# Kernel tuning notes

Measured on AMD Instinct MI355X. Metric: run time of the kernel, lower is better.

Reference implementation:

```python
import jax, jax.numpy as jnp
import numpy as np

N_NODES = 100000
N_EDGES = 1600000
D_IN = 128
D_HID = 128
D_OUT = 16


def gcn_conv(x, W, b, src, dst, deg_inv_sqrt, deg_inv):
    # PyG GCNConv: transform then normalized aggregate with self-loops.
    h = x @ W  # [N, H]
    norm = deg_inv_sqrt[src] * deg_inv_sqrt[dst]  # [E]
    msg = h[src] * norm[:, None]  # [E, H] gather
    agg = jax.ops.segment_sum(msg, dst, num_segments=N_NODES)  # scatter-add
    agg = agg + h * deg_inv[:, None]  # self-loop term (weight deg^-1)
    return agg + b


def setup_inputs() -> dict:
    key = jax.random.key(0)
    ks = jax.random.split(key, 10)
    x = jax.random.normal(ks[0], (N_NODES, D_IN), dtype=jnp.float32)
    edge_index = jax.random.randint(ks[1], (2, N_EDGES), 0, N_NODES)
    s = 1.0 / np.sqrt(D_IN)
    sh = 1.0 / np.sqrt(D_HID)
    W0 = jax.random.uniform(ks[2], (D_IN, D_HID), jnp.float32, -s, s)
    b0 = jnp.zeros((D_HID,), jnp.float32)
    W1 = jax.random.uniform(ks[3], (D_HID, D_HID), jnp.float32, -sh, sh)
    b1 = jnp.zeros((D_HID,), jnp.float32)
    W2 = jax.random.uniform(ks[4], (D_HID, D_HID), jnp.float32, -sh, sh)
    b2 = jnp.zeros((D_HID,), jnp.float32)
    Wr = jax.random.uniform(ks[5], (D_HID, D_OUT), jnp.float32, -sh, sh)
    br = jax.random.uniform(ks[6], (D_OUT,), jnp.float32, -sh, sh)
    return {"x": x, "edge_index": edge_index, "W0": W0, "b0": b0,
            "W1": W1, "b1": b1, "W2": W2, "b2": b2, "Wr": Wr, "br": br}


def reference(x, edge_index, W0, b0, W1, b1, W2, b2, Wr, br):
    src, dst = edge_index[0], edge_index[1]
    # degree with self-loops: deg[i] = 1 + indegree(i)
    deg = jax.ops.segment_sum(jnp.ones((N_EDGES,), x.dtype), dst,
                              num_segments=N_NODES) + 1.0
    deg_inv_sqrt = deg ** -0.5
    deg_inv = 1.0 / deg
    h = x
    for W, b in ((W0, b0), (W1, b1), (W2, b2)):
        h = gcn_conv(h, W, b, src, dst, deg_inv_sqrt, deg_inv)
        h = jax.nn.relu(h)  # dropout is identity at inference
    out = h @ Wr + br
    return jax.nn.sigmoid(out) * 0.8 + 0.1
```

## Files before the change

### kernel.cpp

```cpp
#include <hip/hip_runtime.h>
#include <math.h>

#define N_NODES 100000
#define N_EDGES 1600000
#define NBUCKET 782
#define EB      256
#define EPB     6250

typedef __attribute__((ext_vector_type(8))) __bf16 bf16x8;
typedef __attribute__((ext_vector_type(4))) float  f32x4;


static __device__ __forceinline__ unsigned short f2bf(float f) {
    unsigned int u = __float_as_uint(f);
    unsigned int r = (u + 0x7FFFu + ((u >> 16) & 1u)) >> 16;
    return (unsigned short)r;
}
static __device__ __forceinline__ float bf2f(unsigned short h) {
    return __uint_as_float(((unsigned int)h) << 16);
}


__global__ __launch_bounds__(256) void xconv_kernel(const float* __restrict__ X,
                                                    unsigned short* __restrict__ Xb) {
    int i = (blockIdx.x * 256 + threadIdx.x) * 4;
    float4 v = *(const float4*)&X[i];
    unsigned int p0 = (unsigned int)f2bf(v.x) | ((unsigned int)f2bf(v.y) << 16);
    unsigned int p1 = (unsigned int)f2bf(v.z) | ((unsigned int)f2bf(v.w) << 16);
    *(uint2*)&Xb[i] = make_uint2(p0, p1);
}

__global__ void wconv_kernel(const float* __restrict__ W, unsigned short* __restrict__ Wt) {
    int n = blockIdx.x;
    int k = threadIdx.x;
    Wt[n * 128 + k] = f2bf(W[k * 128 + n]);
}


__global__ __launch_bounds__(256) void hist_kernel(const int* __restrict__ dst,
                                                   int* __restrict__ hist ) {
    __shared__ int h[NBUCKET];
    int tid = threadIdx.x;
    for (int b = tid; b < NBUCKET; b += 256) h[b] = 0;
    __syncthreads();
    int base = blockIdx.x * EPB;
    for (int i = tid; i < EPB; i += 256)
        atomicAdd(&h[dst[base + i] >> 7], 1);
    __syncthreads();
    int* hrow = hist + (size_t)blockIdx.x * NBUCKET;
    for (int b = tid; b < NBUCKET; b += 256) hrow[b] = h[b];
}

__global__ __launch_bounds__(256) void scan_hist_kernel(const int* __restrict__ hist,
                                                        int* __restrict__ blkoffT,
                                                        int* __restrict__ btotal) {
    __shared__ int s[256];
    int b = blockIdx.x;
    int k = threadIdx.x;
    int v = hist[(size_t)k * NBUCKET + b];
    s[k] = v;
    __syncthreads();
    for (int off = 1; off < 256; off <<= 1) {
        int t = 0;
        if (k >= off) t = s[k - off];
        __syncthreads();
        s[k] += t;
        __syncthreads();
    }
    blkoffT[(size_t)b * 256 + k] = s[k] - v;
    if (k == 255) btotal[b] = s[255];
}

__global__ __launch_bounds__(256) void bucket_scan_kernel(const int* __restrict__ btotal,
                                                          int* __restrict__ bucket_start) {
    __shared__ int cs[256];
    int tid = threadIdx.x;
    int base = tid * 4;
    int v[4];
    int sum = 0;
#pragma unroll
    for (int q = 0; q < 4; q++) {
        int idx = base + q;
        v[q] = (idx < NBUCKET) ? btotal[idx] : 0;
        sum += v[q];
    }
    cs[tid] = sum;
    __syncthreads();
    for (int off = 1; off < 256; off <<= 1) {
        int t = 0;
        if (tid >= off) t = cs[tid - off];
        __syncthreads();
        cs[tid] += t;
        __syncthreads();
    }
    int run = cs[tid] - sum;
#pragma unroll
    for (int q = 0; q < 4; q++) {
        int idx = base + q;
        if (idx < NBUCKET + 1) bucket_start[idx] = run;
        run += v[q];
    }
}

__global__ __launch_bounds__(256) void scatter_kernel(const int* __restrict__ src,
                                                      const int* __restrict__ dst,
                                                      const int* __restrict__ blkoffT,
                                                      const int* __restrict__ bucket_start,
                                                      int* __restrict__ pairs) {
    __shared__ int cur[NBUCKET];
    int tid = threadIdx.x;
    for (int b = tid; b < NBUCKET; b += 256)
        cur[b] = bucket_start[b] + blkoffT[(size_t)b * 256 + blockIdx.x];
    __syncthreads();
    int base = blockIdx.x * EPB;
    for (int i = tid; i < EPB; i += 256) {
        int d = dst[base + i];
        int s = src[base + i];
        int pos = atomicAdd(&cur[d >> 7], 1);
        pairs[pos] = s | ((d & 127) << 20);
    }
}

__global__ __launch_bounds__(256) void build_csr_kernel(const int* __restrict__ pairs,
                                                        const int* __restrict__ bucket_start,
                                                        int* __restrict__ rowstart,
                                                        int* __restrict__ counts,
                                                        float* __restrict__ dis,
                                                        int* __restrict__ csr_src) {
    __shared__ int lcnt[128];
    __shared__ int lsc[128];
    __shared__ int lcur[128];
    int tid = threadIdx.x;
    int b = blockIdx.x;
    int node_base = b * 128;
    if (tid < 128) lcnt[tid] = 0;
    __syncthreads();
    int rs = bucket_start[b];
    int re = bucket_start[b + 1];
    for (int e = rs + tid; e < re; e += 256)
        atomicAdd(&lcnt[pairs[e] >> 20], 1);
    __syncthreads();
    if (tid < 128) lsc[tid] = lcnt[tid];
    __syncthreads();
    for (int off = 1; off < 128; off <<= 1) {
        int t = 0;
        if (tid < 128 && tid >= off) t = lsc[tid - off];
        __syncthreads();
        if (tid < 128) lsc[tid] += t;
        __syncthreads();
    }
    if (tid < 128) {
        int node = node_base + tid;
        if (node < N_NODES) {
            int startg = rs + lsc[tid] - lcnt[tid];
            rowstart[node] = startg;
            counts[node]   = lcnt[tid];
            dis[node]      = rsqrtf((float)(lcnt[tid] + 1));
            lcur[tid]      = startg;
        }
    }
    __syncthreads();
    for (int e = rs + tid; e < re; e += 256) {
        int v = pairs[e];
        int pos = atomicAdd(&lcur[v >> 20], 1);
        csr_src[pos] = v & 0xFFFFF;
    }
}


__global__ __launch_bounds__(256) void gemm_mfma_kernel(const unsigned short* __restrict__ Xb,
                                                        const unsigned short* __restrict__ Wt,
                                                        const float* __restrict__ dis,
                                                        unsigned short* __restrict__ Yb) {
    __shared__ unsigned short Xs[128 * 128];
    __shared__ unsigned short Ws[128 * 128];
    int tid = threadIdx.x;
    int rowBase = blockIdx.x * 128;

    {
        int srow = tid >> 1;
        int sk0  = (tid & 1) * 64;
        bool ok = (rowBase + srow) < N_NODES;
        const unsigned short* xsrc = Xb + (size_t)(rowBase + srow) * 128 + sk0;
        const unsigned short* wsrc = Wt + (size_t)srow * 128 + sk0;
#pragma unroll
        for (int i = 0; i < 8; i++) {
            int k = sk0 + i * 8;
            uint4 xv = ok ? *(const uint4*)(xsrc + i * 8) : make_uint4(0, 0, 0, 0);
            uint4 wv = *(const uint4*)(wsrc + i * 8);
            int eo = (srow * 128 + k) ^ ((srow & 7) << 3);
            *(uint4*)&Xs[eo] = xv;
            *(uint4*)&Ws[eo] = wv;
        }
    }
    __syncthreads();

    int lane = tid & 63;
    int wv_  = tid >> 6;
    int wrow = wv_ * 32;
    int lr   = lane & 15;
    int loct = lane >> 4;

    f32x4 acc[2][8];
#pragma unroll
    for (int a = 0; a < 2; a++)
#pragma unroll
        for (int b = 0; b < 8; b++) acc[a][b] = (f32x4){0.f, 0.f, 0.f, 0.f};

#pragma unroll
    for (int s = 0; s < 4; s++) {
        int kb = s * 32 + loct * 8;
        bf16x8 afr[2];
#pragma unroll
        for (int t2 = 0; t2 < 2; t2++) {
            int row = wrow + t2 * 16 + lr;
            int eo = (row * 128 + kb) ^ ((row & 7) << 3);
            afr[t2] = *(const bf16x8*)&Xs[eo];
        }
#pragma unroll
        for (int tc = 0; tc < 8; tc++) {
            int col = tc * 16 + lr;
            int eo = (col * 128 + kb) ^ ((col & 7) << 3);
            bf16x8 bfr = *(const bf16x8*)&Ws[eo];
            acc[0][tc] = __builtin_amdgcn_mfma_f32_16x16x32_bf16(afr[0], bfr, acc[0][tc], 0, 0, 0);
            acc[1][tc] = __builtin_amdgcn_mfma_f32_16x16x32_bf16(afr[1], bfr, acc[1][tc], 0, 0, 0);
        }
    }

#pragma unroll
    for (int t2 = 0; t2 < 2; t2++) {
        int rbase = rowBase + wrow + t2 * 16 + (lane >> 4) * 4;
        float sc[4];
#pragma unroll
        for (int r = 0; r < 4; r++)
            sc[r] = (rbase + r < N_NODES) ? dis[rbase + r] : 0.f;
#pragma unroll
        for (int tc = 0; tc < 8; tc++) {
            int col = tc * 16 + lr;
#pragma unroll
            for (int r = 0; r < 4; r++) {
                int row = rbase + r;
                if (row < N_NODES)
                    Yb[(size_t)row * 128 + col] = f2bf(acc[t2][tc][r] * sc[r]);
            }
        }
    }
}


__global__ __launch_bounds__(256) void aggregate_kernel(const unsigned short* __restrict__ Hs,
                                                        const float* __restrict__ dis,
                                                        const int* __restrict__ rowstart,
                                                        const int* __restrict__ counts,
                                                        const int* __restrict__ csr_src,
                                                        const float* __restrict__ bias,
                                                        unsigned int* __restrict__ OutU) {
    int node = blockIdx.x * 4 + (threadIdx.x >> 6);
    node = __builtin_amdgcn_readfirstlane(node);
    int lane = threadIdx.x & 63;
    if (node >= N_NODES) return;
    int c0 = lane * 2;

    unsigned int ow = *(const unsigned int*)&Hs[(size_t)node * 128 + c0];
    float accx = bf2f((unsigned short)(ow & 0xffffu));
    float accy = bf2f((unsigned short)(ow >> 16));

    int start = rowstart[node];
    int cnt   = counts[node];
    int end = start + cnt;
    int j = start;

    for (; j + 7 < end; j += 8) {
        int s0 = __builtin_nontemporal_load(&csr_src[j]);
        int s1 = __builtin_nontemporal_load(&csr_src[j + 1]);
        int s2 = __builtin_nontemporal_load(&csr_src[j + 2]);
        int s3 = __builtin_nontemporal_load(&csr_src[j + 3]);
        int s4 = __builtin_nontemporal_load(&csr_src[j + 4]);
        int s5 = __builtin_nontemporal_load(&csr_src[j + 5]);
        int s6 = __builtin_nontemporal_load(&csr_src[j + 6]);
        int s7 = __builtin_nontemporal_load(&csr_src[j + 7]);
        unsigned int w0 = *(const unsigned int*)&Hs[(size_t)s0 * 128 + c0];
        unsigned int w1 = *(const unsigned int*)&Hs[(size_t)s1 * 128 + c0];
        unsigned int w2 = *(const unsigned int*)&Hs[(size_t)s2 * 128 + c0];
        unsigned int w3 = *(const unsigned int*)&Hs[(size_t)s3 * 128 + c0];
        unsigned int w4 = *(const unsigned int*)&Hs[(size_t)s4 * 128 + c0];
        unsigned int w5 = *(const unsigned int*)&Hs[(size_t)s5 * 128 + c0];
        unsigned int w6 = *(const unsigned int*)&Hs[(size_t)s6 * 128 + c0];
        unsigned int w7 = *(const unsigned int*)&Hs[(size_t)s7 * 128 + c0];
        accx += ((bf2f((unsigned short)(w0 & 0xffffu)) + bf2f((unsigned short)(w1 & 0xffffu)))
               + (bf2f((unsigned short)(w2 & 0xffffu)) + bf2f((unsigned short)(w3 & 0xffffu))))
              + ((bf2f((unsigned short)(w4 & 0xffffu)) + bf2f((unsigned short)(w5 & 0xffffu)))
               + (bf2f((unsigned short)(w6 & 0xffffu)) + bf2f((unsigned short)(w7 & 0xffffu))));
        accy += ((bf2f((unsigned short)(w0 >> 16)) + bf2f((unsigned short)(w1 >> 16)))
               + (bf2f((unsigned short)(w2 >> 16)) + bf2f((unsigned short)(w3 >> 16))))
              + ((bf2f((unsigned short)(w4 >> 16)) + bf2f((unsigned short)(w5 >> 16)))
               + (bf2f((unsigned short)(w6 >> 16)) + bf2f((unsigned short)(w7 >> 16))));
    }
    for (; j + 1 < end; j += 2) {
        int s0 = __builtin_nontemporal_load(&csr_src[j]);
        int s1 = __builtin_nontemporal_load(&csr_src[j + 1]);
        unsigned int w0 = *(const unsigned int*)&Hs[(size_t)s0 * 128 + c0];
        unsigned int w1 = *(const unsigned int*)&Hs[(size_t)s1 * 128 + c0];
        accx += bf2f((unsigned short)(w0 & 0xffffu)) + bf2f((unsigned short)(w1 & 0xffffu));
        accy += bf2f((unsigned short)(w0 >> 16)) + bf2f((unsigned short)(w1 >> 16));
    }
    if (j < end) {
        int s0 = __builtin_nontemporal_load(&csr_src[j]);
        unsigned int w0 = *(const unsigned int*)&Hs[(size_t)s0 * 128 + c0];
        accx += bf2f((unsigned short)(w0 & 0xffffu));
        accy += bf2f((unsigned short)(w0 >> 16));
    }

    float dsi = dis[node];
    float2 bb = *(const float2*)&bias[c0];
    float rx = fmaxf(fmaf(accx, dsi, bb.x), 0.f);
    float ry = fmaxf(fmaf(accy, dsi, bb.y), 0.f);
    unsigned int pk = (unsigned int)f2bf(rx) | ((unsigned int)f2bf(ry) << 16);
    __builtin_nontemporal_store(pk, &OutU[(size_t)node * 64 + lane]);
}


__global__ __launch_bounds__(256) void final_kernel(const unsigned short* __restrict__ Hb,
                                                    const float* __restrict__ Wr,
                                                    const float* __restrict__ br,
                                                    float* __restrict__ out) {
    __shared__ float hs[16][132];
    __shared__ float ws[128][16];
    int tid = threadIdx.x;
    int rowBase = blockIdx.x * 16;
    {
#pragma unroll
        for (int q = 0; q < 4; q++) {
            int idx = q * 256 + tid;
            int r  = idx >> 6;
            int kp = (idx & 63) * 2;
            unsigned int w = *(const unsigned int*)&Hb[(size_t)(rowBase + r) * 128 + kp];
            hs[r][kp]     = bf2f((unsigned short)(w & 0xffffu));
            hs[r][kp + 1] = bf2f((unsigned short)(w >> 16));
        }
#pragma unroll
        for (int q = 0; q < 8; q++) {
            int idx = q * 256 + tid;
            ws[idx >> 4][idx & 15] = Wr[idx];
        }
    }
    __syncthreads();
    int row = tid >> 4;
    int c   = tid & 15;
    float acc = br[c];
#pragma unroll
    for (int k = 0; k < 128; k++)
        acc = fmaf(hs[row][k], ws[k][c], acc);
    int grow = rowBase + row;
    float sg = 1.f / (1.f + expf(-acc));
    out[(size_t)grow * 16 + c] = 0.8f * sg + 0.1f;
}


extern "C" void kernel_launch(void* const* d_in, const int* in_sizes, int n_in,
                              void* d_out, int out_size, void* d_ws, size_t ws_size,
                              hipStream_t stream) {
    const float* x  = (const float*)d_in[0];
    const int*   ei = (const int*)d_in[1];
    const int*   src = ei;
    const int*   dst = ei + N_EDGES;
    const float* W0 = (const float*)d_in[2];
    const float* b0 = (const float*)d_in[3];
    const float* W1 = (const float*)d_in[4];
    const float* b1 = (const float*)d_in[5];
    const float* W2 = (const float*)d_in[6];
    const float* b2 = (const float*)d_in[7];
    const float* Wr = (const float*)d_in[8];
    const float* br = (const float*)d_in[9];
    float* out = (float*)d_out;

    char* ws = (char*)d_ws;
    size_t off = 0;
    auto take = [&](size_t bytes) {
        char* p = ws + off;
        off += (bytes + 255) & ~(size_t)255;
        return p;
    };
    unsigned short* hAb      = (unsigned short*)take((size_t)N_NODES * 128 * 2);
    unsigned short* hBs      = (unsigned short*)take((size_t)N_NODES * 128 * 2);
    unsigned short* xb       = (unsigned short*)take((size_t)N_NODES * 128 * 2);
    unsigned short* Wt       = (unsigned short*)take(128 * 128 * 2);
    int*            counts   = (int*)take((size_t)N_NODES * 4);
    int*            rowstart = (int*)take((size_t)N_NODES * 4);
    float*          dis      = (float*)take((size_t)N_NODES * 4);
    int*            csr_src  = (int*)take((size_t)N_EDGES * 4);
    int*            pairs    = (int*)take((size_t)N_EDGES * 4);
    int*            hist     = (int*)take((size_t)EB * NBUCKET * 4);
    int*            blkoffT  = (int*)take((size_t)NBUCKET * EB * 4);
    int*            btotal   = (int*)take(1024 * 4);
    int*            bstart   = (int*)take(1024 * 4);
    (void)ws_size; (void)in_sizes; (void)n_in; (void)out_size;

    xconv_kernel<<<12500, 256, 0, stream>>>(x, xb);

    hist_kernel<<<EB, 256, 0, stream>>>(dst, hist);
    scan_hist_kernel<<<NBUCKET, 256, 0, stream>>>(hist, blkoffT, btotal);
    bucket_scan_kernel<<<1, 256, 0, stream>>>(btotal, bstart);
    scatter_kernel<<<EB, 256, 0, stream>>>(src, dst, blkoffT, bstart, pairs);
    build_csr_kernel<<<NBUCKET, 256, 0, stream>>>(pairs, bstart, rowstart, counts, dis, csr_src);

    const float* Wl[3] = {W0, W1, W2};
    const float* bl[3] = {b0, b1, b2};
    const unsigned short* hin = xb;
    for (int l = 0; l < 3; l++) {
        wconv_kernel<<<128, 128, 0, stream>>>(Wl[l], Wt);
        gemm_mfma_kernel<<<(N_NODES + 127) / 128, 256, 0, stream>>>(hin, Wt, dis, hBs);
        aggregate_kernel<<<N_NODES / 4, 256, 0, stream>>>(hBs, dis, rowstart, counts,
                                                          csr_src, bl[l], (unsigned int*)hAb);
        hin = hAb;
    }
    final_kernel<<<N_NODES / 16, 256, 0, stream>>>(hAb, Wr, br, out);
}
```

Before: 478.5 us.

## Fuse fp32-to-bf16 input conversion into first GEMM and drop LDS staging

Removes the separate x conversion kernel and its bf16 buffer by having the first-layer GEMM read fp32 rows directly and convert them to bf16 in registers. It also drops LDS staging for both operands, so the MFMA fragments are loaded straight from global memory, with W reused through the cache. This saves one kernel launch and a full write-plus-read of the converted input. The cost is less coalesced per-lane global loads and repeated W reads served by L1/L2 instead of shared memory.

```diff
diff --git a/kernel.cpp b/kernel.cpp
--- a/kernel.cpp
+++ b/kernel.cpp
@@ -18,16 +18,6 @@
 }
 static __device__ __forceinline__ float bf2f(unsigned short h) {
     return __uint_as_float(((unsigned int)h) << 16);
-}
-
-
-__global__ __launch_bounds__(256) void xconv_kernel(const float* __restrict__ X,
-                                                    unsigned short* __restrict__ Xb) {
-    int i = (blockIdx.x * 256 + threadIdx.x) * 4;
-    float4 v = *(const float4*)&X[i];
-    unsigned int p0 = (unsigned int)f2bf(v.x) | ((unsigned int)f2bf(v.y) << 16);
-    unsigned int p1 = (unsigned int)f2bf(v.z) | ((unsigned int)f2bf(v.w) << 16);
-    *(uint2*)&Xb[i] = make_uint2(p0, p1);
 }
 
 __global__ void wconv_kernel(const float* __restrict__ W, unsigned short* __restrict__ Wt) {
@@ -168,39 +158,22 @@
 }
 
 
-__global__ __launch_bounds__(256) void gemm_mfma_kernel(const unsigned short* __restrict__ Xb,
+template <bool FP32IN>
+__global__ __launch_bounds__(256) void gemm_mfma_kernel(const void* __restrict__ Xin,
                                                         const unsigned short* __restrict__ Wt,
                                                         const float* __restrict__ dis,
                                                         unsigned short* __restrict__ Yb) {
-    __shared__ unsigned short Xs[128 * 128];
-    __shared__ unsigned short Ws[128 * 128];
     int tid = threadIdx.x;
     int rowBase = blockIdx.x * 128;
-
-    {
-        int srow = tid >> 1;
-        int sk0  = (tid & 1) * 64;
-        bool ok = (rowBase + srow) < N_NODES;
-        const unsigned short* xsrc = Xb + (size_t)(rowBase + srow) * 128 + sk0;
-        const unsigned short* wsrc = Wt + (size_t)srow * 128 + sk0;
-#pragma unroll
-        for (int i = 0; i < 8; i++) {
-            int k = sk0 + i * 8;
-            uint4 xv = ok ? *(const uint4*)(xsrc + i * 8) : make_uint4(0, 0, 0, 0);
-            uint4 wv = *(const uint4*)(wsrc + i * 8);
-            int eo = (srow * 128 + k) ^ ((srow & 7) << 3);
-            *(uint4*)&Xs[eo] = xv;
-            *(uint4*)&Ws[eo] = wv;
-        }
-    }
-    __syncthreads();
-
     int lane = tid & 63;
     int wv_  = tid >> 6;
     int wrow = wv_ * 32;
     int lr   = lane & 15;
     int loct = lane >> 4;
 
+    const float*          Xf = (const float*)Xin;
+    const unsigned short* Xb = (const unsigned short*)Xin;
+
     f32x4 acc[2][8];
 #pragma unroll
     for (int a = 0; a < 2; a++)
@@ -213,15 +186,31 @@
         bf16x8 afr[2];
 #pragma unroll
         for (int t2 = 0; t2 < 2; t2++) {
-            int row = wrow + t2 * 16 + lr;
-            int eo = (row * 128 + kb) ^ ((row & 7) << 3);
-            afr[t2] = *(const bf16x8*)&Xs[eo];
+            int row = rowBase + wrow + t2 * 16 + lr;
+            if (row < N_NODES) {
+                if (FP32IN) {
+                    float4 v0 = *(const float4*)&Xf[(size_t)row * 128 + kb];
+                    float4 v1 = *(const float4*)&Xf[(size_t)row * 128 + kb + 4];
+                    union { unsigned short u[8]; bf16x8 v; } cv;
+                    cv.u[0] = f2bf(v0.x); cv.u[1] = f2bf(v0.y);
+                    cv.u[2] = f2bf(v0.z); cv.u[3] = f2bf(v0.w);
+                    cv.u[4] = f2bf(v1.x); cv.u[5] = f2bf(v1.y);
+                    cv.u[6] = f2bf(v1.z); cv.u[7] = f2bf(v1.w);
+                    afr[t2] = cv.v;
+                } else {
+                    afr[t2] = *(const bf16x8*)&Xb[(size_t)row * 128 + kb];
+                }
+            } else {
+                union { unsigned short u[8]; bf16x8 v; } z;
+#pragma unroll
+                for (int j = 0; j < 8; j++) z.u[j] = 0;
+                afr[t2] = z.v;
+            }
         }
 #pragma unroll
         for (int tc = 0; tc < 8; tc++) {
             int col = tc * 16 + lr;
-            int eo = (col * 128 + kb) ^ ((col & 7) << 3);
-            bf16x8 bfr = *(const bf16x8*)&Ws[eo];
+            bf16x8 bfr = *(const bf16x8*)&Wt[(size_t)col * 128 + kb];
             acc[0][tc] = __builtin_amdgcn_mfma_f32_16x16x32_bf16(afr[0], bfr, acc[0][tc], 0, 0, 0);
             acc[1][tc] = __builtin_amdgcn_mfma_f32_16x16x32_bf16(afr[1], bfr, acc[1][tc], 0, 0, 0);
         }
@@ -383,7 +372,6 @@
     };
     unsigned short* hAb      = (unsigned short*)take((size_t)N_NODES * 128 * 2);
     unsigned short* hBs      = (unsigned short*)take((size_t)N_NODES * 128 * 2);
-    unsigned short* xb       = (unsigned short*)take((size_t)N_NODES * 128 * 2);
     unsigned short* Wt       = (unsigned short*)take(128 * 128 * 2);
     int*            counts   = (int*)take((size_t)N_NODES * 4);
     int*            rowstart = (int*)take((size_t)N_NODES * 4);
@@ -396,8 +384,6 @@
     int*            bstart   = (int*)take(1024 * 4);
     (void)ws_size; (void)in_sizes; (void)n_in; (void)out_size;
 
-    xconv_kernel<<<12500, 256, 0, stream>>>(x, xb);
-
     hist_kernel<<<EB, 256, 0, stream>>>(dst, hist);
     scan_hist_kernel<<<NBUCKET, 256, 0, stream>>>(hist, blkoffT, btotal);
     bucket_scan_kernel<<<1, 256, 0, stream>>>(btotal, bstart);
@@ -406,13 +392,15 @@
 
     const float* Wl[3] = {W0, W1, W2};
     const float* bl[3] = {b0, b1, b2};
-    const unsigned short* hin = xb;
+    int gemmBlocks = (N_NODES + 127) / 128;
     for (int l = 0; l < 3; l++) {
         wconv_kernel<<<128, 128, 0, stream>>>(Wl[l], Wt);
-        gemm_mfma_kernel<<<(N_NODES + 127) / 128, 256, 0, stream>>>(hin, Wt, dis, hBs);
+        if (l == 0)
+            gemm_mfma_kernel<true><<<gemmBlocks, 256, 0, stream>>>(x, Wt, dis, hBs);
+        else
+            gemm_mfma_kernel<false><<<gemmBlocks, 256, 0, stream>>>(hAb, Wt, dis, hBs);
         aggregate_kernel<<<N_NODES / 4, 256, 0, stream>>>(hBs, dis, rowstart, counts,
                                                           csr_src, bl[l], (unsigned int*)hAb);
-        hin = hAb;
     }
     final_kernel<<<N_NODES / 16, 256, 0, stream>>>(hAb, Wr, br, out);
 }
```

Measured after the change: 470.0 us. Within noise of the previous version (-1.8%).
